# Kernel optimization log

Hardware: AMD Instinct MI355X
Metric: run time of the kernel (lower is better)

Reference implementation:

```python
import jax, jax.numpy as jnp
import numpy as np

DIM = 128

def _rope_tables(seq_len, dim, dtype):
    inv_freq = 1.0 / (10000.0 ** (jnp.arange(0, dim, 2, dtype=jnp.float32) / dim))
    t = jnp.arange(seq_len, dtype=jnp.float32)
    freqs = t[:, None] * inv_freq[None, :]          # [S, dim/2]
    emb = jnp.concatenate([freqs, freqs], axis=-1)  # [S, dim]
    return jnp.cos(emb).astype(dtype), jnp.sin(emb).astype(dtype)

def _rotate_half(x):
    x1, x2 = jnp.split(x, 2, axis=-1)
    return jnp.concatenate([-x2, x1], axis=-1)

def _apply_rope(x, cos, sin):
    return x * cos + _rotate_half(x) * sin

def setup_inputs() -> dict:
    key = jax.random.key(0)
    kq, kk, kv = jax.random.split(key, 3)
    B, S, D = 4, 4096, DIM
    return {
        "Q": jax.random.normal(kq, (B, S, D), dtype=jnp.float32),
        "K": jax.random.normal(kk, (B, S, D), dtype=jnp.float32),
        "V": jax.random.normal(kv, (B, S, D), dtype=jnp.float32),
    }

def reference(Q, K, V):
    B, S, D = Q.shape
    cos, sin = _rope_tables(S, D, Q.dtype)  # [S, D], broadcast over batch
    Qr = _apply_rope(Q, cos, sin)
    Kr = _apply_rope(K, cos, sin)
    energy = jnp.einsum('bqd,bkd->bqk', Qr, Kr)  # [B, S, S]
    # causal mask: zero out strictly-upper triangle (no softmax)
    causal = jnp.tril(jnp.ones((S, S), dtype=bool))
    energy = jnp.where(causal, energy, jnp.zeros((), dtype=energy.dtype))
    return jnp.einsum('bqk,bkd->bqd', energy, V)
```

## Files before the change

### kernel.cpp

```cpp
#include <hip/hip_runtime.h>
#include <hip/hip_bf16.h>

#define S_LEN 4096
#define DIM   128
#define NB    4
#define L_CHUNK 128
#define NCH   (S_LEN / L_CHUNK)
#define NHC   (2 * NCH)
#define ROPE_BLKS (NB * S_LEN / 4)
#define TR_BLKS   (NB * S_LEN / 64)
#define NQT   (S_LEN / 256)
#define CH_FB 3

typedef __bf16 bf16_t;
typedef __attribute__((ext_vector_type(4)))  float        f32x4;
typedef __attribute__((ext_vector_type(8)))  __bf16       bf16x8;
typedef __attribute__((ext_vector_type(16))) float        f32x16;
typedef __attribute__((ext_vector_type(4)))  unsigned int u32x4;

#define MFMA32(a, b, c) __builtin_amdgcn_mfma_f32_32x32x16_bf16((a), (b), (c), 0, 0, 0)
#define CVTPK(d, a, b) asm("v_cvt_pk_bf16_f32 %0, %1, %2" : "=v"(d) : "v"(a), "v"(b))
#define PSWAP(d, s)    asm("v_permlane32_swap_b32 %0, %1" : "+v"(d), "+v"(s))

__device__ __forceinline__ unsigned swzo(int row, int colByte) {
    return (unsigned)(row * 256 + (colByte ^ ((row & 15) << 4)));
}
__device__ __forceinline__ unsigned swz64(int row, int colByte) {
    return (unsigned)(row * 128 + (colByte ^ ((row & 7) << 4)));
}

__device__ __forceinline__ void cvt_swap(const f32x16& s, unsigned int w[8]) {
    CVTPK(w[0], s[0],  s[1]);  CVTPK(w[1], s[2],  s[3]);
    CVTPK(w[2], s[4],  s[5]);  CVTPK(w[3], s[6],  s[7]);
    CVTPK(w[4], s[8],  s[9]);  CVTPK(w[5], s[10], s[11]);
    CVTPK(w[6], s[12], s[13]); CVTPK(w[7], s[14], s[15]);
    PSWAP(w[0], w[2]); PSWAP(w[1], w[3]);
    PSWAP(w[4], w[6]); PSWAP(w[5], w[7]);
}

__launch_bounds__(256, 2)
__global__ void mega_prep_kernel(const float* __restrict__ Q,
                                 const float* __restrict__ K,
                                 const float* __restrict__ V,
                                 bf16_t* __restrict__ Qr,
                                 bf16_t* __restrict__ Kr,
                                 bf16_t* __restrict__ Vt,
                                 bf16_t* __restrict__ Gh) {
    __shared__ bf16_t KsT[128 * 64];
    __shared__ bf16_t VsT[128 * 64];
    int b  = blockIdx.x >> 6;
    int hc = blockIdx.x & 63;
    int k0 = hc * 64;
    int tid = threadIdx.x, w = tid >> 6, lane = tid & 63;
    int lr = lane & 31, lg = lane >> 5;

    {
        int srow = tid >> 2;
        int j    = tid & 3;
        int s    = k0 + srow;
        size_t base = ((size_t)b * S_LEN + s) * DIM;
        f32x4 ql[4], qh[4], kl[4], vl[4], vh[4], kh[4];
        #pragma unroll
        for (int u = 0; u < 4; ++u) {
            ql[u] = *(const f32x4*)(Q + base + 16 * j + 4 * u);
            qh[u] = *(const f32x4*)(Q + base + 64 + 16 * j + 4 * u);
            kl[u] = *(const f32x4*)(K + base + 16 * j + 4 * u);
            kh[u] = *(const f32x4*)(K + base + 64 + 16 * j + 4 * u);
            vl[u] = *(const f32x4*)(V + base + 16 * j + 4 * u);
            vh[u] = *(const f32x4*)(V + base + 64 + 16 * j + 4 * u);
        }
        bf16_t oql[16], oqh[16], okl[16], okh[16];
        #pragma unroll
        for (int e = 0; e < 16; ++e) {
            int i = 16 * j + e;
            float ex      = -(float)i * (13.287712379549449f / 64.0f);
            float inv_rev = exp2f(ex) * 0.15915494309189535f;
            float rev = (float)s * inv_rev;
            float fr  = rev - floorf(rev);
            float c  = __builtin_amdgcn_cosf(fr);
            float sn = __builtin_amdgcn_sinf(fr);
            float q1 = ql[e >> 2][e & 3], q2 = qh[e >> 2][e & 3];
            float k1 = kl[e >> 2][e & 3], k2 = kh[e >> 2][e & 3];
            oql[e] = (bf16_t)(q1 * c - q2 * sn);
            oqh[e] = (bf16_t)(q2 * c + q1 * sn);
            okl[e] = (bf16_t)(k1 * c - k2 * sn);
            okh[e] = (bf16_t)(k2 * c + k1 * sn);
        }
        #pragma unroll
        for (int hlf = 0; hlf < 2; ++hlf) {
            *(bf16x8*)(Qr + base + 16 * j + 8 * hlf)      = *(bf16x8*)&oql[8 * hlf];
            *(bf16x8*)(Qr + base + 64 + 16 * j + 8 * hlf) = *(bf16x8*)&oqh[8 * hlf];
            *(bf16x8*)(Kr + base + 16 * j + 8 * hlf)      = *(bf16x8*)&okl[8 * hlf];
            *(bf16x8*)(Kr + base + 64 + 16 * j + 8 * hlf) = *(bf16x8*)&okh[8 * hlf];
        }
        #pragma unroll
        for (int e = 0; e < 16; ++e) {
            int dk = 16 * j + e;
            *(bf16_t*)((char*)KsT + swz64(dk,      srow * 2)) = okl[e];
            *(bf16_t*)((char*)KsT + swz64(dk + 64, srow * 2)) = okh[e];
            *(bf16_t*)((char*)VsT + swz64(dk,      srow * 2)) = (bf16_t)vl[e >> 2][e & 3];
            *(bf16_t*)((char*)VsT + swz64(dk + 64, srow * 2)) = (bf16_t)vh[e >> 2][e & 3];
        }
    }
    __syncthreads();

    f32x16 acc[4];
    #pragma unroll
    for (int db = 0; db < 4; ++db)
        #pragma unroll
        for (int r = 0; r < 16; ++r) acc[db][r] = 0.f;

    #pragma unroll
    for (int sI = 0; sI < 4; ++sI) {
        bf16x8 af = *(const bf16x8*)((const char*)VsT +
            swz64(32 * w + lr, (sI * 16 + lg * 8) * 2));
        #pragma unroll
        for (int db = 0; db < 4; ++db) {
            bf16x8 bfr = *(const bf16x8*)((const char*)KsT +
                swz64(32 * db + lr, (sI * 16 + lg * 8) * 2));
            acc[db] = MFMA32(af, bfr, acc[db]);
        }
    }
    bf16_t* Gc = Gh + ((size_t)b * NHC + hc) * DIM * DIM;
    #pragma unroll
    for (int db = 0; db < 4; ++db)
        #pragma unroll
        for (int r = 0; r < 16; ++r) {
            int dv = 32 * w + (r & 3) + ((r >> 2) << 3) + (lg << 2);
            Gc[(size_t)dv * DIM + 32 * db + lr] = (bf16_t)acc[db][r];
        }

    #pragma unroll
    for (int m = 0; m < 4; ++m) {
        int idx  = tid + 256 * m;
        int dv   = idx >> 3;
        int slot = idx & 7;
        bf16x8 v = *(const bf16x8*)((const char*)VsT + swz64(dv, slot * 16));
        *(bf16x8*)(Vt + ((size_t)b * DIM + dv) * S_LEN + k0 + slot * 8) = v;
    }
}

__global__ void stage2_kernel(const bf16_t* __restrict__ Gh, bf16_t* __restrict__ Gp) {
    int b = blockIdx.x >> 6;
    int p = (blockIdx.x & 63) * 128 + threadIdx.x;
    const bf16_t* ph = Gh + (size_t)b * NHC * DIM * DIM + (size_t)p * 2;
    bf16_t* pp = Gp + (size_t)b * NCH * DIM * DIM + (size_t)p * 2;
    float rlo = 0.f, rhi = 0.f;
    #pragma unroll
    for (int c = 0; c < NCH; ++c) {
        unsigned s = (unsigned)__builtin_bit_cast(unsigned short, (bf16_t)rlo) |
                     ((unsigned)__builtin_bit_cast(unsigned short, (bf16_t)rhi) << 16);
        *(unsigned*)(pp + (size_t)c * DIM * DIM) = s;
        unsigned u0 = *(const unsigned*)(ph + (size_t)(2 * c) * DIM * DIM);
        unsigned u1 = *(const unsigned*)(ph + (size_t)(2 * c + 1) * DIM * DIM);
        rlo += __builtin_bit_cast(float, u0 << 16) + __builtin_bit_cast(float, u1 << 16);
        rhi += __builtin_bit_cast(float, u0 & 0xffff0000u) +
               __builtin_bit_cast(float, u1 & 0xffff0000u);
    }
}

__launch_bounds__(256, 1)
__global__ void stage3_kernel(const bf16_t* __restrict__ Qr,
                              const bf16_t* __restrict__ Kr,
                              const bf16_t* __restrict__ Vt,
                              const bf16_t* __restrict__ Gp,
                              float* __restrict__ Out) {
    __shared__ bf16_t Ks[128 * 128];
    __shared__ bf16_t Vs[64 * 128];
    int b  = blockIdx.x >> 6;
    int c  = (blockIdx.x >> 1) & 31;
    int dh = blockIdx.x & 1;
    int tid = threadIdx.x, w = tid >> 6, lane = tid & 63;
    int lr = lane & 31, lg = lane >> 5;
    int q0 = c * L_CHUNK;
    const bf16_t* Qb = Qr + (size_t)b * S_LEN * DIM;
    const bf16_t* Kb = Kr + (size_t)b * S_LEN * DIM;
    const bf16_t* Vb = Vt + (size_t)b * DIM * S_LEN;
    const bf16_t* Gb = Gp + ((size_t)b * NCH + c) * DIM * DIM;

    bf16x8 qf[8];
    #pragma unroll
    for (int s2 = 0; s2 < 8; ++s2)
        qf[s2] = *(const bf16x8*)(Qb + (size_t)(q0 + 32 * w + lr) * DIM
                                  + s2 * 16 + lg * 8);

    #pragma unroll
    for (int j = 0; j < 8; ++j) {
        int idx = tid + j * 256;
        int row = idx >> 4, slot = idx & 15;
        u32x4 kd = *(const u32x4*)(Kb + (size_t)(q0 + row) * DIM + slot * 8);
        *(u32x4*)((char*)Ks + swzo(row, slot * 16)) = kd;
    }
    #pragma unroll
    for (int j = 0; j < 4; ++j) {
        int idx = tid + j * 256;
        int row = idx >> 4, slot = idx & 15;
        u32x4 vd = *(const u32x4*)(Vb + (size_t)(64 * dh + row) * S_LEN + q0 + slot * 8);
        *(u32x4*)((char*)Vs + swzo(row, slot * 16)) = vd;
    }
    __syncthreads();

    f32x16 acc[2];
    #pragma unroll
    for (int i = 0; i < 2; ++i)
        #pragma unroll
        for (int r = 0; r < 16; ++r) acc[i][r] = 0.f;

    if (c > 0) {
        #pragma unroll
        for (int s2 = 0; s2 < 8; ++s2) {
            #pragma unroll
            for (int i = 0; i < 2; ++i) {
                bf16x8 gfr = *(const bf16x8*)(Gb +
                    (size_t)(64 * dh + 32 * i + lr) * DIM + s2 * 16 + lg * 8);
                acc[i] = MFMA32(qf[s2], gfr, acc[i]);
            }
        }
    }

    for (int g = 0; g <= w; ++g) {
        int ksub = g * 32;
        f32x16 sa;
        #pragma unroll
        for (int r = 0; r < 16; ++r) sa[r] = 0.f;
        #pragma unroll
        for (int s2 = 0; s2 < 8; ++s2) {
            bf16x8 af = *(const bf16x8*)((const char*)Ks +
                swzo(ksub + lr, (s2 * 16 + lg * 8) * 2));
            sa = MFMA32(af, qf[s2], sa);
        }
        if (g == w) {
            #pragma unroll
            for (int r = 0; r < 16; ++r) {
                int crow = (r & 3) + ((r >> 2) << 3) + (lg << 2);
                sa[r] = (crow > lr) ? 0.f : sa[r];
            }
        }
        unsigned int wv[8];
        cvt_swap(sa, wv);
        u32x4 tA = {wv[0], wv[1], wv[2], wv[3]};
        u32x4 tB = {wv[4], wv[5], wv[6], wv[7]};
        bf16x8 pA = __builtin_bit_cast(bf16x8, tA);
        bf16x8 pB = __builtin_bit_cast(bf16x8, tB);
        #pragma unroll
        for (int i = 0; i < 2; ++i) {
            bf16x8 v0 = *(const bf16x8*)((const char*)Vs +
                swzo(32 * i + lr, (ksub + lg * 8) * 2));
            bf16x8 v1 = *(const bf16x8*)((const char*)Vs +
                swzo(32 * i + lr, (ksub + 16 + lg * 8) * 2));
            acc[i] = MFMA32(pA, v0, acc[i]);
            acc[i] = MFMA32(pB, v1, acc[i]);
        }
    }

    float* Ob = Out + (size_t)b * S_LEN * DIM;
    #pragma unroll
    for (int i = 0; i < 2; ++i)
        #pragma unroll
        for (int r = 0; r < 16; ++r) {
            int q = q0 + 32 * w + (r & 3) + ((r >> 2) << 3) + (lg << 2);
            int d = 64 * dh + 32 * i + lr;
            Ob[(size_t)q * DIM + d] = acc[i][r];
        }
}

__global__ void prep_fb_kernel(const float* __restrict__ Q,
                               const float* __restrict__ K,
                               const float* __restrict__ V,
                               bf16_t* __restrict__ Qr,
                               bf16_t* __restrict__ Kr,
                               bf16_t* __restrict__ Vt) {
    int bid = blockIdx.x;
    int t   = threadIdx.x;
    if (bid < ROPE_BLKS) {
        int i   = t & 63;
        int row = bid * 4 + (t >> 6);
        int s   = row & (S_LEN - 1);
        size_t base = (size_t)row * DIM;
        float e       = -(float)i * (13.287712379549449f / 64.0f);
        float inv_rev = exp2f(e) * 0.15915494309189535f;
        float rev = (float)s * inv_rev;
        float fr  = rev - floorf(rev);
        float c  = __builtin_amdgcn_cosf(fr);
        float sn = __builtin_amdgcn_sinf(fr);
        float q1 = Q[base + i], q2 = Q[base + i + 64];
        float k1 = K[base + i], k2 = K[base + i + 64];
        Qr[base + i]      = (bf16_t)(q1 * c - q2 * sn);
        Qr[base + i + 64] = (bf16_t)(q2 * c + q1 * sn);
        Kr[base + i]      = (bf16_t)(k1 * c - k2 * sn);
        Kr[base + i + 64] = (bf16_t)(k2 * c + k1 * sn);
    } else {
        int idx = bid - ROPE_BLKS;
        int b   = idx >> 6;
        int s0  = (idx & 63) * 64;
        int d   = t >> 1;
        int sh  = (t & 1) * 32;
        const float* vb = V + (size_t)b * S_LEN * DIM;
        bf16_t* ob = Vt + ((size_t)b * DIM + d) * S_LEN;
        #pragma unroll
        for (int j8 = 0; j8 < 4; ++j8) {
            bf16x8 u;
            #pragma unroll
            for (int e2 = 0; e2 < 8; ++e2) {
                int s = s0 + sh + j8 * 8 + e2;
                u[e2] = (bf16_t)vb[(size_t)s * DIM + d];
            }
            *(bf16x8*)(ob + s0 + sh + j8 * 8) = u;
        }
    }
}

__launch_bounds__(256, 2)
__global__ void attn_fb_kernel(const bf16_t* __restrict__ Qr,
                               const bf16_t* __restrict__ Kr,
                               const bf16_t* __restrict__ Vt,
                               float* __restrict__ Out) {
    __shared__ bf16_t Kt[128 * 128];
    __shared__ bf16_t Vl[128 * 128];
    int b = blockIdx.x & 3;
    int t = blockIdx.x >> 2;
    int qt = 0, c0 = 0;
    for (int i2 = NQT - 1; i2 >= 0; --i2) {
        int n = (2 * (i2 + 1) + CH_FB - 1) / CH_FB;
        if (t < n) { qt = i2; c0 = t; break; }
        t -= n;
    }
    int nkt   = 2 * (qt + 1);
    int kt_lo = c0 * CH_FB;
    int kt_hi = min(kt_lo + CH_FB, nkt);
    bool single = ((nkt + CH_FB - 1) / CH_FB) == 1;

    int tid = threadIdx.x, w = tid >> 6, lane = tid & 63;
    int lr = lane & 31, lg = lane >> 5;
    int qw = qt * 256 + w * 64;
    const bf16_t* Qb = Qr + (size_t)b * S_LEN * DIM;
    const bf16_t* Kb = Kr + (size_t)b * S_LEN * DIM;
    const bf16_t* Vb = Vt + (size_t)b * DIM * S_LEN;

    bf16x8 qf[2][8];
    #pragma unroll
    for (int qb = 0; qb < 2; ++qb)
        #pragma unroll
        for (int s2 = 0; s2 < 8; ++s2)
            qf[qb][s2] = *(const bf16x8*)(Qb + (size_t)(qw + qb * 32 + lr) * DIM
                                          + s2 * 16 + lg * 8);
    f32x16 acc[2][4];
    #pragma unroll
    for (int qb = 0; qb < 2; ++qb)
        #pragma unroll
        for (int db = 0; db < 4; ++db)
            #pragma unroll
            for (int r = 0; r < 16; ++r) acc[qb][db][r] = 0.f;

    for (int kt = kt_lo; kt < kt_hi; ++kt) {
        int kbase = kt * 128;
        #pragma unroll
        for (int j = 0; j < 8; ++j) {
            int idx = tid + j * 256;
            int row = idx >> 4, slot = idx & 15;
            u32x4 kd = *(const u32x4*)(Kb + (size_t)(kbase + row) * DIM + slot * 8);
            *(u32x4*)((char*)Kt + swzo(row, slot * 16)) = kd;
            u32x4 vd = *(const u32x4*)(Vb + (size_t)row * S_LEN + kbase + slot * 8);
            *(u32x4*)((char*)Vl + swzo(row, slot * 16)) = vd;
        }
        __syncthreads();
        #pragma unroll
        for (int kb = 0; kb < 4; ++kb) {
            int ksub = kb * 32;
            int kmin = kbase + ksub;
            if (kmin > qw + 63) break;
            bool do0 = (kmin <= qw + 31);
            f32x16 s0, s1;
            #pragma unroll
            for (int r = 0; r < 16; ++r) { s0[r] = 0.f; s1[r] = 0.f; }
            #pragma unroll
            for (int h = 0; h < 2; ++h) {
                bf16x8 af[4];
                #pragma unroll
                for (int s2 = 0; s2 < 4; ++s2)
                    af[s2] = *(const bf16x8*)((const char*)Kt +
                        swzo(ksub + lr, (h * 64 + s2 * 16 + lg * 8) * 2));
                #pragma unroll
                for (int s2 = 0; s2 < 4; ++s2) {
                    if (do0) s0 = MFMA32(af[s2], qf[0][h * 4 + s2], s0);
                    s1 = MFMA32(af[s2], qf[1][h * 4 + s2], s1);
                }
            }
            if (kmin + 31 > qw) {
                #pragma unroll
                for (int r = 0; r < 16; ++r) {
                    int kg = kmin + (r & 3) + ((r >> 2) << 3) + (lg << 2);
                    s0[r] = (kg > qw + lr)      ? 0.f : s0[r];
                    s1[r] = (kg > qw + 32 + lr) ? 0.f : s1[r];
                }
            }
            unsigned int w0[8], w1[8];
            cvt_swap(s0, w0);
            cvt_swap(s1, w1);
            u32x4 t00 = {w0[0], w0[1], w0[2], w0[3]};
            u32x4 t01 = {w0[4], w0[5], w0[6], w0[7]};
            u32x4 t10 = {w1[0], w1[1], w1[2], w1[3]};
            u32x4 t11 = {w1[4], w1[5], w1[6], w1[7]};
            bf16x8 p00 = __builtin_bit_cast(bf16x8, t00);
            bf16x8 p01 = __builtin_bit_cast(bf16x8, t01);
            bf16x8 p10 = __builtin_bit_cast(bf16x8, t10);
            bf16x8 p11 = __builtin_bit_cast(bf16x8, t11);
            #pragma unroll
            for (int db = 0; db < 4; ++db) {
                bf16x8 vb0 = *(const bf16x8*)((const char*)Vl +
                    swzo(db * 32 + lr, (ksub + lg * 8) * 2));
                bf16x8 vb1 = *(const bf16x8*)((const char*)Vl +
                    swzo(db * 32 + lr, (ksub + 16 + lg * 8) * 2));
                if (do0) {
                    acc[0][db] = MFMA32(p00, vb0, acc[0][db]);
                    acc[0][db] = MFMA32(p01, vb1, acc[0][db]);
                }
                acc[1][db] = MFMA32(p10, vb0, acc[1][db]);
                acc[1][db] = MFMA32(p11, vb1, acc[1][db]);
            }
        }
        __syncthreads();
    }
    float* Ob = Out + (size_t)b * S_LEN * DIM;
    #pragma unroll
    for (int qb = 0; qb < 2; ++qb)
        #pragma unroll
        for (int db = 0; db < 4; ++db)
            #pragma unroll
            for (int r = 0; r < 16; ++r) {
                int q = qw + qb * 32 + (r & 3) + ((r >> 2) << 3) + (lg << 2);
                int d = db * 32 + lr;
                float v = acc[qb][db][r];
                float* p = Ob + (size_t)q * DIM + d;
                if (single) *p = v; else atomicAdd(p, v);
            }
}

extern "C" void kernel_launch(void* const* d_in, const int* in_sizes, int n_in,
                              void* d_out, int out_size, void* d_ws, size_t ws_size,
                              hipStream_t stream) {
    const float* Q = (const float*)d_in[0];
    const float* K = (const float*)d_in[1];
    const float* V = (const float*)d_in[2];
    float* Out = (float*)d_out;

    size_t plane  = (size_t)NB * S_LEN * DIM * sizeof(bf16_t);
    size_t ghalf  = (size_t)NB * NHC * DIM * DIM * sizeof(bf16_t);
    size_t gpre   = (size_t)NB * NCH * DIM * DIM * sizeof(bf16_t);
    char* wsb = (char*)d_ws;
    bf16_t* Qr = (bf16_t*)wsb;
    bf16_t* Kr = (bf16_t*)(wsb + plane);
    bf16_t* Vt = (bf16_t*)(wsb + 2 * plane);

    if (ws_size >= 3 * plane + ghalf + gpre) {
        bf16_t* Gh = (bf16_t*)(wsb + 3 * plane);
        bf16_t* Gp = (bf16_t*)(wsb + 3 * plane + ghalf);
        mega_prep_kernel<<<NB * NHC, 256, 0, stream>>>(Q, K, V, Qr, Kr, Vt, Gh);
        stage2_kernel<<<NB * 64, 128, 0, stream>>>(Gh, Gp);
        stage3_kernel<<<NB * NCH * 2, 256, 0, stream>>>(Qr, Kr, Vt, Gp, Out);
    } else if (ws_size >= 3 * plane) {
        hipMemsetAsync(d_out, 0, (size_t)NB * S_LEN * DIM * sizeof(float), stream);
        prep_fb_kernel<<<ROPE_BLKS + TR_BLKS, 256, 0, stream>>>(Q, K, V, Qr, Kr, Vt);
        int chunks = 0;
        for (int i = 0; i < NQT; ++i) chunks += (2 * (i + 1) + CH_FB - 1) / CH_FB;
        attn_fb_kernel<<<NB * chunks, 256, 0, stream>>>(Qr, Kr, Vt, Out);
    }
}
```

Measured before the change: 30.06 us.

## Fuse three stage kernels into one cooperative kernel with grid syncs

Merges the prep (RoPE, transpose, per-chunk KᵀV), prefix-sum and attention stages into one cooperative kernel of 256 blocks, using grid.sync between stages instead of separate launches. This removes two kernel launch gaps and tail effects. The prefix-sum stage now handles one bf16 element per thread instead of a packed pair, and launch bounds drop to one block per SM. It relies on cooperative launch support and on all 256 blocks being co-resident.

New measurement: 104.4 us. 3.47x slower.

```diff
diff --git a/kernel.cpp b/kernel.cpp
--- a/kernel.cpp
+++ b/kernel.cpp
@@ -1,5 +1,8 @@
 #include <hip/hip_runtime.h>
 #include <hip/hip_bf16.h>
+#include <hip/hip_cooperative_groups.h>
+
+namespace cg = cooperative_groups;
 
 #define S_LEN 4096
 #define DIM   128
@@ -38,230 +41,231 @@
     PSWAP(w[4], w[6]); PSWAP(w[5], w[7]);
 }
 
-__launch_bounds__(256, 2)
-__global__ void mega_prep_kernel(const float* __restrict__ Q,
+__launch_bounds__(256, 1)
+__global__ void fused_all_kernel(const float* __restrict__ Q,
                                  const float* __restrict__ K,
                                  const float* __restrict__ V,
                                  bf16_t* __restrict__ Qr,
                                  bf16_t* __restrict__ Kr,
                                  bf16_t* __restrict__ Vt,
-                                 bf16_t* __restrict__ Gh) {
-    __shared__ bf16_t KsT[128 * 64];
-    __shared__ bf16_t VsT[128 * 64];
-    int b  = blockIdx.x >> 6;
-    int hc = blockIdx.x & 63;
-    int k0 = hc * 64;
+                                 bf16_t* __restrict__ Gh,
+                                 bf16_t* __restrict__ Gp,
+                                 float* __restrict__ Out) {
+    __shared__ char smem[49152];
+    cg::grid_group grid = cg::this_grid();
+
+    int bid = blockIdx.x;
     int tid = threadIdx.x, w = tid >> 6, lane = tid & 63;
     int lr = lane & 31, lg = lane >> 5;
 
     {
-        int srow = tid >> 2;
-        int j    = tid & 3;
-        int s    = k0 + srow;
-        size_t base = ((size_t)b * S_LEN + s) * DIM;
-        f32x4 ql[4], qh[4], kl[4], vl[4], vh[4], kh[4];
-        #pragma unroll
-        for (int u = 0; u < 4; ++u) {
-            ql[u] = *(const f32x4*)(Q + base + 16 * j + 4 * u);
-            qh[u] = *(const f32x4*)(Q + base + 64 + 16 * j + 4 * u);
-            kl[u] = *(const f32x4*)(K + base + 16 * j + 4 * u);
-            kh[u] = *(const f32x4*)(K + base + 64 + 16 * j + 4 * u);
-            vl[u] = *(const f32x4*)(V + base + 16 * j + 4 * u);
-            vh[u] = *(const f32x4*)(V + base + 64 + 16 * j + 4 * u);
-        }
-        bf16_t oql[16], oqh[16], okl[16], okh[16];
-        #pragma unroll
-        for (int e = 0; e < 16; ++e) {
-            int i = 16 * j + e;
-            float ex      = -(float)i * (13.287712379549449f / 64.0f);
-            float inv_rev = exp2f(ex) * 0.15915494309189535f;
-            float rev = (float)s * inv_rev;
-            float fr  = rev - floorf(rev);
-            float c  = __builtin_amdgcn_cosf(fr);
-            float sn = __builtin_amdgcn_sinf(fr);
-            float q1 = ql[e >> 2][e & 3], q2 = qh[e >> 2][e & 3];
-            float k1 = kl[e >> 2][e & 3], k2 = kh[e >> 2][e & 3];
-            oql[e] = (bf16_t)(q1 * c - q2 * sn);
-            oqh[e] = (bf16_t)(q2 * c + q1 * sn);
-            okl[e] = (bf16_t)(k1 * c - k2 * sn);
-            okh[e] = (bf16_t)(k2 * c + k1 * sn);
-        }
-        #pragma unroll
-        for (int hlf = 0; hlf < 2; ++hlf) {
-            *(bf16x8*)(Qr + base + 16 * j + 8 * hlf)      = *(bf16x8*)&oql[8 * hlf];
-            *(bf16x8*)(Qr + base + 64 + 16 * j + 8 * hlf) = *(bf16x8*)&oqh[8 * hlf];
-            *(bf16x8*)(Kr + base + 16 * j + 8 * hlf)      = *(bf16x8*)&okl[8 * hlf];
-            *(bf16x8*)(Kr + base + 64 + 16 * j + 8 * hlf) = *(bf16x8*)&okh[8 * hlf];
-        }
-        #pragma unroll
-        for (int e = 0; e < 16; ++e) {
-            int dk = 16 * j + e;
-            *(bf16_t*)((char*)KsT + swz64(dk,      srow * 2)) = okl[e];
-            *(bf16_t*)((char*)KsT + swz64(dk + 64, srow * 2)) = okh[e];
-            *(bf16_t*)((char*)VsT + swz64(dk,      srow * 2)) = (bf16_t)vl[e >> 2][e & 3];
-            *(bf16_t*)((char*)VsT + swz64(dk + 64, srow * 2)) = (bf16_t)vh[e >> 2][e & 3];
-        }
-    }
-    __syncthreads();
-
-    f32x16 acc[4];
-    #pragma unroll
-    for (int db = 0; db < 4; ++db)
-        #pragma unroll
-        for (int r = 0; r < 16; ++r) acc[db][r] = 0.f;
-
-    #pragma unroll
-    for (int sI = 0; sI < 4; ++sI) {
-        bf16x8 af = *(const bf16x8*)((const char*)VsT +
-            swz64(32 * w + lr, (sI * 16 + lg * 8) * 2));
-        #pragma unroll
-        for (int db = 0; db < 4; ++db) {
-            bf16x8 bfr = *(const bf16x8*)((const char*)KsT +
-                swz64(32 * db + lr, (sI * 16 + lg * 8) * 2));
-            acc[db] = MFMA32(af, bfr, acc[db]);
-        }
-    }
-    bf16_t* Gc = Gh + ((size_t)b * NHC + hc) * DIM * DIM;
-    #pragma unroll
-    for (int db = 0; db < 4; ++db)
-        #pragma unroll
-        for (int r = 0; r < 16; ++r) {
-            int dv = 32 * w + (r & 3) + ((r >> 2) << 3) + (lg << 2);
-            Gc[(size_t)dv * DIM + 32 * db + lr] = (bf16_t)acc[db][r];
-        }
-
-    #pragma unroll
-    for (int m = 0; m < 4; ++m) {
-        int idx  = tid + 256 * m;
-        int dv   = idx >> 3;
-        int slot = idx & 7;
-        bf16x8 v = *(const bf16x8*)((const char*)VsT + swz64(dv, slot * 16));
-        *(bf16x8*)(Vt + ((size_t)b * DIM + dv) * S_LEN + k0 + slot * 8) = v;
-    }
-}
-
-__global__ void stage2_kernel(const bf16_t* __restrict__ Gh, bf16_t* __restrict__ Gp) {
-    int b = blockIdx.x >> 6;
-    int p = (blockIdx.x & 63) * 128 + threadIdx.x;
-    const bf16_t* ph = Gh + (size_t)b * NHC * DIM * DIM + (size_t)p * 2;
-    bf16_t* pp = Gp + (size_t)b * NCH * DIM * DIM + (size_t)p * 2;
-    float rlo = 0.f, rhi = 0.f;
-    #pragma unroll
-    for (int c = 0; c < NCH; ++c) {
-        unsigned s = (unsigned)__builtin_bit_cast(unsigned short, (bf16_t)rlo) |
-                     ((unsigned)__builtin_bit_cast(unsigned short, (bf16_t)rhi) << 16);
-        *(unsigned*)(pp + (size_t)c * DIM * DIM) = s;
-        unsigned u0 = *(const unsigned*)(ph + (size_t)(2 * c) * DIM * DIM);
-        unsigned u1 = *(const unsigned*)(ph + (size_t)(2 * c + 1) * DIM * DIM);
-        rlo += __builtin_bit_cast(float, u0 << 16) + __builtin_bit_cast(float, u1 << 16);
-        rhi += __builtin_bit_cast(float, u0 & 0xffff0000u) +
-               __builtin_bit_cast(float, u1 & 0xffff0000u);
-    }
-}
-
-__launch_bounds__(256, 1)
-__global__ void stage3_kernel(const bf16_t* __restrict__ Qr,
-                              const bf16_t* __restrict__ Kr,
-                              const bf16_t* __restrict__ Vt,
-                              const bf16_t* __restrict__ Gp,
-                              float* __restrict__ Out) {
-    __shared__ bf16_t Ks[128 * 128];
-    __shared__ bf16_t Vs[64 * 128];
-    int b  = blockIdx.x >> 6;
-    int c  = (blockIdx.x >> 1) & 31;
-    int dh = blockIdx.x & 1;
-    int tid = threadIdx.x, w = tid >> 6, lane = tid & 63;
-    int lr = lane & 31, lg = lane >> 5;
-    int q0 = c * L_CHUNK;
-    const bf16_t* Qb = Qr + (size_t)b * S_LEN * DIM;
-    const bf16_t* Kb = Kr + (size_t)b * S_LEN * DIM;
-    const bf16_t* Vb = Vt + (size_t)b * DIM * S_LEN;
-    const bf16_t* Gb = Gp + ((size_t)b * NCH + c) * DIM * DIM;
-
-    bf16x8 qf[8];
-    #pragma unroll
-    for (int s2 = 0; s2 < 8; ++s2)
-        qf[s2] = *(const bf16x8*)(Qb + (size_t)(q0 + 32 * w + lr) * DIM
-                                  + s2 * 16 + lg * 8);
-
-    #pragma unroll
-    for (int j = 0; j < 8; ++j) {
-        int idx = tid + j * 256;
-        int row = idx >> 4, slot = idx & 15;
-        u32x4 kd = *(const u32x4*)(Kb + (size_t)(q0 + row) * DIM + slot * 8);
-        *(u32x4*)((char*)Ks + swzo(row, slot * 16)) = kd;
-    }
-    #pragma unroll
-    for (int j = 0; j < 4; ++j) {
-        int idx = tid + j * 256;
-        int row = idx >> 4, slot = idx & 15;
-        u32x4 vd = *(const u32x4*)(Vb + (size_t)(64 * dh + row) * S_LEN + q0 + slot * 8);
-        *(u32x4*)((char*)Vs + swzo(row, slot * 16)) = vd;
-    }
-    __syncthreads();
-
-    f32x16 acc[2];
-    #pragma unroll
-    for (int i = 0; i < 2; ++i)
-        #pragma unroll
-        for (int r = 0; r < 16; ++r) acc[i][r] = 0.f;
-
-    if (c > 0) {
-        #pragma unroll
-        for (int s2 = 0; s2 < 8; ++s2) {
+        bf16_t* KsT = (bf16_t*)smem;
+        bf16_t* VsT = (bf16_t*)(smem + 16384);
+        int b  = bid >> 6;
+        int hc = bid & 63;
+        int k0 = hc * 64;
+        {
+            int srow = tid >> 2;
+            int j    = tid & 3;
+            int s    = k0 + srow;
+            size_t base = ((size_t)b * S_LEN + s) * DIM;
+            f32x4 ql[4], qh[4], kl[4], vl[4], vh[4], kh[4];
+            #pragma unroll
+            for (int u = 0; u < 4; ++u) {
+                ql[u] = *(const f32x4*)(Q + base + 16 * j + 4 * u);
+                qh[u] = *(const f32x4*)(Q + base + 64 + 16 * j + 4 * u);
+                kl[u] = *(const f32x4*)(K + base + 16 * j + 4 * u);
+                kh[u] = *(const f32x4*)(K + base + 64 + 16 * j + 4 * u);
+                vl[u] = *(const f32x4*)(V + base + 16 * j + 4 * u);
+                vh[u] = *(const f32x4*)(V + base + 64 + 16 * j + 4 * u);
+            }
+            bf16_t oql[16], oqh[16], okl[16], okh[16];
+            #pragma unroll
+            for (int e = 0; e < 16; ++e) {
+                int i = 16 * j + e;
+                float ex      = -(float)i * (13.287712379549449f / 64.0f);
+                float inv_rev = exp2f(ex) * 0.15915494309189535f;
+                float rev = (float)s * inv_rev;
+                float fr  = rev - floorf(rev);
+                float c  = __builtin_amdgcn_cosf(fr);
+                float sn = __builtin_amdgcn_sinf(fr);
+                float q1 = ql[e >> 2][e & 3], q2 = qh[e >> 2][e & 3];
+                float k1 = kl[e >> 2][e & 3], k2 = kh[e >> 2][e & 3];
+                oql[e] = (bf16_t)(q1 * c - q2 * sn);
+                oqh[e] = (bf16_t)(q2 * c + q1 * sn);
+                okl[e] = (bf16_t)(k1 * c - k2 * sn);
+                okh[e] = (bf16_t)(k2 * c + k1 * sn);
+            }
+            #pragma unroll
+            for (int hlf = 0; hlf < 2; ++hlf) {
+                *(bf16x8*)(Qr + base + 16 * j + 8 * hlf)      = *(bf16x8*)&oql[8 * hlf];
+                *(bf16x8*)(Qr + base + 64 + 16 * j + 8 * hlf) = *(bf16x8*)&oqh[8 * hlf];
+                *(bf16x8*)(Kr + base + 16 * j + 8 * hlf)      = *(bf16x8*)&okl[8 * hlf];
+                *(bf16x8*)(Kr + base + 64 + 16 * j + 8 * hlf) = *(bf16x8*)&okh[8 * hlf];
+            }
+            #pragma unroll
+            for (int e = 0; e < 16; ++e) {
+                int dk = 16 * j + e;
+                *(bf16_t*)((char*)KsT + swz64(dk,      srow * 2)) = okl[e];
+                *(bf16_t*)((char*)KsT + swz64(dk + 64, srow * 2)) = okh[e];
+                *(bf16_t*)((char*)VsT + swz64(dk,      srow * 2)) = (bf16_t)vl[e >> 2][e & 3];
+                *(bf16_t*)((char*)VsT + swz64(dk + 64, srow * 2)) = (bf16_t)vh[e >> 2][e & 3];
+            }
+        }
+        __syncthreads();
+
+        f32x16 acc[4];
+        #pragma unroll
+        for (int db = 0; db < 4; ++db)
+            #pragma unroll
+            for (int r = 0; r < 16; ++r) acc[db][r] = 0.f;
+
+        #pragma unroll
+        for (int sI = 0; sI < 4; ++sI) {
+            bf16x8 af = *(const bf16x8*)((const char*)VsT +
+                swz64(32 * w + lr, (sI * 16 + lg * 8) * 2));
+            #pragma unroll
+            for (int db = 0; db < 4; ++db) {
+                bf16x8 bfr = *(const bf16x8*)((const char*)KsT +
+                    swz64(32 * db + lr, (sI * 16 + lg * 8) * 2));
+                acc[db] = MFMA32(af, bfr, acc[db]);
+            }
+        }
+        bf16_t* Gc = Gh + ((size_t)b * NHC + hc) * DIM * DIM;
+        #pragma unroll
+        for (int db = 0; db < 4; ++db)
+            #pragma unroll
+            for (int r = 0; r < 16; ++r) {
+                int dv = 32 * w + (r & 3) + ((r >> 2) << 3) + (lg << 2);
+                Gc[(size_t)dv * DIM + 32 * db + lr] = (bf16_t)acc[db][r];
+            }
+
+        #pragma unroll
+        for (int m = 0; m < 4; ++m) {
+            int idx  = tid + 256 * m;
+            int dv   = idx >> 3;
+            int slot = idx & 7;
+            bf16x8 v = *(const bf16x8*)((const char*)VsT + swz64(dv, slot * 16));
+            *(bf16x8*)(Vt + ((size_t)b * DIM + dv) * S_LEN + k0 + slot * 8) = v;
+        }
+    }
+
+    grid.sync();
+
+    {
+        int col = bid * 256 + tid;
+        int b   = col >> 14;
+        int p   = col & 16383;
+        const bf16_t* ph = Gh + (size_t)b * NHC * DIM * DIM + p;
+        bf16_t* pp = Gp + (size_t)b * NCH * DIM * DIM + p;
+        float run = 0.f;
+        #pragma unroll
+        for (int c = 0; c < NCH; ++c) {
+            pp[(size_t)c * DIM * DIM] = (bf16_t)run;
+            run += (float)ph[(size_t)(2 * c) * DIM * DIM] +
+                   (float)ph[(size_t)(2 * c + 1) * DIM * DIM];
+        }
+    }
+
+    grid.sync();
+
+    {
+        bf16_t* Ks = (bf16_t*)smem;
+        bf16_t* Vs = (bf16_t*)(smem + 32768);
+        int b  = bid >> 6;
+        int c  = (bid >> 1) & 31;
+        int dh = bid & 1;
+        int q0 = c * L_CHUNK;
+        const bf16_t* Qb = Qr + (size_t)b * S_LEN * DIM;
+        const bf16_t* Kb = Kr + (size_t)b * S_LEN * DIM;
+        const bf16_t* Vb = Vt + (size_t)b * DIM * S_LEN;
+        const bf16_t* Gb = Gp + ((size_t)b * NCH + c) * DIM * DIM;
+
+        bf16x8 qf[8];
+        #pragma unroll
+        for (int s2 = 0; s2 < 8; ++s2)
+            qf[s2] = *(const bf16x8*)(Qb + (size_t)(q0 + 32 * w + lr) * DIM
+                                      + s2 * 16 + lg * 8);
+
+        #pragma unroll
+        for (int j = 0; j < 8; ++j) {
+            int idx = tid + j * 256;
+            int row = idx >> 4, slot = idx & 15;
+            u32x4 kd = *(const u32x4*)(Kb + (size_t)(q0 + row) * DIM + slot * 8);
+            *(u32x4*)((char*)Ks + swzo(row, slot * 16)) = kd;
+        }
+        #pragma unroll
+        for (int j = 0; j < 4; ++j) {
+            int idx = tid + j * 256;
+            int row = idx >> 4, slot = idx & 15;
+            u32x4 vd = *(const u32x4*)(Vb + (size_t)(64 * dh + row) * S_LEN + q0 + slot * 8);
+            *(u32x4*)((char*)Vs + swzo(row, slot * 16)) = vd;
+        }
+        __syncthreads();
+
+        f32x16 acc[2];
+        #pragma unroll
+        for (int i = 0; i < 2; ++i)
+            #pragma unroll
+            for (int r = 0; r < 16; ++r) acc[i][r] = 0.f;
+
+        if (c > 0) {
+            #pragma unroll
+            for (int s2 = 0; s2 < 8; ++s2) {
+                #pragma unroll
+                for (int i = 0; i < 2; ++i) {
+                    bf16x8 gfr = *(const bf16x8*)(Gb +
+                        (size_t)(64 * dh + 32 * i + lr) * DIM + s2 * 16 + lg * 8);
+                    acc[i] = MFMA32(qf[s2], gfr, acc[i]);
+                }
+            }
+        }
+
+        for (int g = 0; g <= w; ++g) {
+            int ksub = g * 32;
+            f32x16 sa;
+            #pragma unroll
+            for (int r = 0; r < 16; ++r) sa[r] = 0.f;
+            #pragma unroll
+            for (int s2 = 0; s2 < 8; ++s2) {
+                bf16x8 af = *(const bf16x8*)((const char*)Ks +
+                    swzo(ksub + lr, (s2 * 16 + lg * 8) * 2));
+                sa = MFMA32(af, qf[s2], sa);
+            }
+            if (g == w) {
+                #pragma unroll
+                for (int r = 0; r < 16; ++r) {
+                    int crow = (r & 3) + ((r >> 2) << 3) + (lg << 2);
+                    sa[r] = (crow > lr) ? 0.f : sa[r];
+                }
+            }
+            unsigned int wv[8];
+            cvt_swap(sa, wv);
+            u32x4 tA = {wv[0], wv[1], wv[2], wv[3]};
+            u32x4 tB = {wv[4], wv[5], wv[6], wv[7]};
+            bf16x8 pA = __builtin_bit_cast(bf16x8, tA);
+            bf16x8 pB = __builtin_bit_cast(bf16x8, tB);
             #pragma unroll
             for (int i = 0; i < 2; ++i) {
-                bf16x8 gfr = *(const bf16x8*)(Gb +
-                    (size_t)(64 * dh + 32 * i + lr) * DIM + s2 * 16 + lg * 8);
-                acc[i] = MFMA32(qf[s2], gfr, acc[i]);
-            }
-        }
-    }
-
-    for (int g = 0; g <= w; ++g) {
-        int ksub = g * 32;
-        f32x16 sa;
-        #pragma unroll
-        for (int r = 0; r < 16; ++r) sa[r] = 0.f;
-        #pragma unroll
-        for (int s2 = 0; s2 < 8; ++s2) {
-            bf16x8 af = *(const bf16x8*)((const char*)Ks +
-                swzo(ksub + lr, (s2 * 16 + lg * 8) * 2));
-            sa = MFMA32(af, qf[s2], sa);
-        }
-        if (g == w) {
+                bf16x8 v0 = *(const bf16x8*)((const char*)Vs +
+                    swzo(32 * i + lr, (ksub + lg * 8) * 2));
+                bf16x8 v1 = *(const bf16x8*)((const char*)Vs +
+                    swzo(32 * i + lr, (ksub + 16 + lg * 8) * 2));
+                acc[i] = MFMA32(pA, v0, acc[i]);
+                acc[i] = MFMA32(pB, v1, acc[i]);
+            }
+        }
+
+        float* Ob = Out + (size_t)b * S_LEN * DIM;
+        #pragma unroll
+        for (int i = 0; i < 2; ++i)
             #pragma unroll
             for (int r = 0; r < 16; ++r) {
-                int crow = (r & 3) + ((r >> 2) << 3) + (lg << 2);
-                sa[r] = (crow > lr) ? 0.f : sa[r];
-            }
-        }
-        unsigned int wv[8];
-        cvt_swap(sa, wv);
-        u32x4 tA = {wv[0], wv[1], wv[2], wv[3]};
-        u32x4 tB = {wv[4], wv[5], wv[6], wv[7]};
-        bf16x8 pA = __builtin_bit_cast(bf16x8, tA);
-        bf16x8 pB = __builtin_bit_cast(bf16x8, tB);
-        #pragma unroll
-        for (int i = 0; i < 2; ++i) {
-            bf16x8 v0 = *(const bf16x8*)((const char*)Vs +
-                swzo(32 * i + lr, (ksub + lg * 8) * 2));
-            bf16x8 v1 = *(const bf16x8*)((const char*)Vs +
-                swzo(32 * i + lr, (ksub + 16 + lg * 8) * 2));
-            acc[i] = MFMA32(pA, v0, acc[i]);
-            acc[i] = MFMA32(pB, v1, acc[i]);
-        }
-    }
-
-    float* Ob = Out + (size_t)b * S_LEN * DIM;
-    #pragma unroll
-    for (int i = 0; i < 2; ++i)
-        #pragma unroll
-        for (int r = 0; r < 16; ++r) {
-            int q = q0 + 32 * w + (r & 3) + ((r >> 2) << 3) + (lg << 2);
-            int d = 64 * dh + 32 * i + lr;
-            Ob[(size_t)q * DIM + d] = acc[i][r];
-        }
+                int q = q0 + 32 * w + (r & 3) + ((r >> 2) << 3) + (lg << 2);
+                int d = 64 * dh + 32 * i + lr;
+                Ob[(size_t)q * DIM + d] = acc[i][r];
+            }
+    }
 }
 
 __global__ void prep_fb_kernel(const float* __restrict__ Q,
@@ -455,9 +459,10 @@
     if (ws_size >= 3 * plane + ghalf + gpre) {
         bf16_t* Gh = (bf16_t*)(wsb + 3 * plane);
         bf16_t* Gp = (bf16_t*)(wsb + 3 * plane + ghalf);
-        mega_prep_kernel<<<NB * NHC, 256, 0, stream>>>(Q, K, V, Qr, Kr, Vt, Gh);
-        stage2_kernel<<<NB * 64, 128, 0, stream>>>(Gh, Gp);
-        stage3_kernel<<<NB * NCH * 2, 256, 0, stream>>>(Qr, Kr, Vt, Gp, Out);
+        void* kargs[] = {(void*)&Q, (void*)&K, (void*)&V, (void*)&Qr, (void*)&Kr,
+                         (void*)&Vt, (void*)&Gh, (void*)&Gp, (void*)&Out};
+        hipLaunchCooperativeKernel((const void*)fused_all_kernel,
+                                   dim3(NB * NHC), dim3(256), kargs, 0, stream);
     } else if (ws_size >= 3 * plane) {
         hipMemsetAsync(d_out, 0, (size_t)NB * S_LEN * DIM * sizeof(float), stream);
         prep_fb_kernel<<<ROPE_BLKS + TR_BLKS, 256, 0, stream>>>(Q, K, V, Qr, Kr, Vt);
```

## Fuse RoPE of Q/K into consumer kernels and stage prefix state in LDS

Applied to the files above, without the earlier changes.

The prep kernel no longer writes rotated bf16 Q and K planes to the workspace. Instead stage3 reads fp32 Q and K directly and applies RoPE on the fly, and the G kernel recomputes rotated K locally. This removes the round-trip writes and reads of two bf16 planes. In exchange it adds an extra fp32 read of K and Q plus duplicated sin/cos work. Stage3 also copies its prefix-state slice into swizzled LDS once, rather than reading it from global memory inside the MFMA loop, which costs extra LDS.

Measured after the change: 31.96 us. +6.3%, slower.

```diff
diff --git a/kernel.cpp b/kernel.cpp
--- a/kernel.cpp
+++ b/kernel.cpp
@@ -38,14 +38,20 @@
     PSWAP(w[4], w[6]); PSWAP(w[5], w[7]);
 }
 
+__device__ __forceinline__ void ropesc(int seq, int i, float& cc, float& ss) {
+    float ex      = -(float)i * (13.287712379549449f / 64.0f);
+    float inv_rev = exp2f(ex) * 0.15915494309189535f;
+    float rev = (float)seq * inv_rev;
+    float fr  = rev - floorf(rev);
+    cc = __builtin_amdgcn_cosf(fr);
+    ss = __builtin_amdgcn_sinf(fr);
+}
+
 __launch_bounds__(256, 2)
-__global__ void mega_prep_kernel(const float* __restrict__ Q,
-                                 const float* __restrict__ K,
-                                 const float* __restrict__ V,
-                                 bf16_t* __restrict__ Qr,
-                                 bf16_t* __restrict__ Kr,
-                                 bf16_t* __restrict__ Vt,
-                                 bf16_t* __restrict__ Gh) {
+__global__ void g_kernel(const float* __restrict__ K,
+                         const float* __restrict__ V,
+                         bf16_t* __restrict__ Vt,
+                         bf16_t* __restrict__ Gh) {
     __shared__ bf16_t KsT[128 * 64];
     __shared__ bf16_t VsT[128 * 64];
     int b  = blockIdx.x >> 6;
@@ -59,45 +65,25 @@
         int j    = tid & 3;
         int s    = k0 + srow;
         size_t base = ((size_t)b * S_LEN + s) * DIM;
-        f32x4 ql[4], qh[4], kl[4], vl[4], vh[4], kh[4];
+        f32x4 kl[4], kh[4], vl[4], vh[4];
         #pragma unroll
         for (int u = 0; u < 4; ++u) {
-            ql[u] = *(const f32x4*)(Q + base + 16 * j + 4 * u);
-            qh[u] = *(const f32x4*)(Q + base + 64 + 16 * j + 4 * u);
             kl[u] = *(const f32x4*)(K + base + 16 * j + 4 * u);
             kh[u] = *(const f32x4*)(K + base + 64 + 16 * j + 4 * u);
             vl[u] = *(const f32x4*)(V + base + 16 * j + 4 * u);
             vh[u] = *(const f32x4*)(V + base + 64 + 16 * j + 4 * u);
         }
-        bf16_t oql[16], oqh[16], okl[16], okh[16];
         #pragma unroll
         for (int e = 0; e < 16; ++e) {
             int i = 16 * j + e;
-            float ex      = -(float)i * (13.287712379549449f / 64.0f);
-            float inv_rev = exp2f(ex) * 0.15915494309189535f;
-            float rev = (float)s * inv_rev;
-            float fr  = rev - floorf(rev);
-            float c  = __builtin_amdgcn_cosf(fr);
-            float sn = __builtin_amdgcn_sinf(fr);
-            float q1 = ql[e >> 2][e & 3], q2 = qh[e >> 2][e & 3];
+            float cc, ssn;
+            ropesc(s, i, cc, ssn);
             float k1 = kl[e >> 2][e & 3], k2 = kh[e >> 2][e & 3];
-            oql[e] = (bf16_t)(q1 * c - q2 * sn);
-            oqh[e] = (bf16_t)(q2 * c + q1 * sn);
-            okl[e] = (bf16_t)(k1 * c - k2 * sn);
-            okh[e] = (bf16_t)(k2 * c + k1 * sn);
-        }
-        #pragma unroll
-        for (int hlf = 0; hlf < 2; ++hlf) {
-            *(bf16x8*)(Qr + base + 16 * j + 8 * hlf)      = *(bf16x8*)&oql[8 * hlf];
-            *(bf16x8*)(Qr + base + 64 + 16 * j + 8 * hlf) = *(bf16x8*)&oqh[8 * hlf];
-            *(bf16x8*)(Kr + base + 16 * j + 8 * hlf)      = *(bf16x8*)&okl[8 * hlf];
-            *(bf16x8*)(Kr + base + 64 + 16 * j + 8 * hlf) = *(bf16x8*)&okh[8 * hlf];
-        }
-        #pragma unroll
-        for (int e = 0; e < 16; ++e) {
-            int dk = 16 * j + e;
-            *(bf16_t*)((char*)KsT + swz64(dk,      srow * 2)) = okl[e];
-            *(bf16_t*)((char*)KsT + swz64(dk + 64, srow * 2)) = okh[e];
+            bf16_t okl = (bf16_t)(k1 * cc - k2 * ssn);
+            bf16_t okh = (bf16_t)(k2 * cc + k1 * ssn);
+            int dk = i;
+            *(bf16_t*)((char*)KsT + swz64(dk,      srow * 2)) = okl;
+            *(bf16_t*)((char*)KsT + swz64(dk + 64, srow * 2)) = okh;
             *(bf16_t*)((char*)VsT + swz64(dk,      srow * 2)) = (bf16_t)vl[e >> 2][e & 3];
             *(bf16_t*)((char*)VsT + swz64(dk + 64, srow * 2)) = (bf16_t)vh[e >> 2][e & 3];
         }
@@ -160,37 +146,75 @@
 }
 
 __launch_bounds__(256, 1)
-__global__ void stage3_kernel(const bf16_t* __restrict__ Qr,
-                              const bf16_t* __restrict__ Kr,
+__global__ void stage3_kernel(const float* __restrict__ Qf,
+                              const float* __restrict__ Kf,
                               const bf16_t* __restrict__ Vt,
                               const bf16_t* __restrict__ Gp,
                               float* __restrict__ Out) {
     __shared__ bf16_t Ks[128 * 128];
     __shared__ bf16_t Vs[64 * 128];
+    __shared__ bf16_t Gs[64 * 128];
     int b  = blockIdx.x >> 6;
     int c  = (blockIdx.x >> 1) & 31;
     int dh = blockIdx.x & 1;
     int tid = threadIdx.x, w = tid >> 6, lane = tid & 63;
     int lr = lane & 31, lg = lane >> 5;
     int q0 = c * L_CHUNK;
-    const bf16_t* Qb = Qr + (size_t)b * S_LEN * DIM;
-    const bf16_t* Kb = Kr + (size_t)b * S_LEN * DIM;
     const bf16_t* Vb = Vt + (size_t)b * DIM * S_LEN;
     const bf16_t* Gb = Gp + ((size_t)b * NCH + c) * DIM * DIM;
 
     bf16x8 qf[8];
-    #pragma unroll
-    for (int s2 = 0; s2 < 8; ++s2)
-        qf[s2] = *(const bf16x8*)(Qb + (size_t)(q0 + 32 * w + lr) * DIM
-                                  + s2 * 16 + lg * 8);
-
-    #pragma unroll
-    for (int j = 0; j < 8; ++j) {
-        int idx = tid + j * 256;
-        int row = idx >> 4, slot = idx & 15;
-        u32x4 kd = *(const u32x4*)(Kb + (size_t)(q0 + row) * DIM + slot * 8);
-        *(u32x4*)((char*)Ks + swzo(row, slot * 16)) = kd;
-    }
+    {
+        int rowg = q0 + 32 * w + lr;
+        const float* Qrow = Qf + ((size_t)b * S_LEN + rowg) * DIM;
+        #pragma unroll
+        for (int s2 = 0; s2 < 8; ++s2) {
+            int c0 = s2 * 16 + lg * 8;
+            f32x4 qa0 = *(const f32x4*)(Qrow + c0);
+            f32x4 qa1 = *(const f32x4*)(Qrow + c0 + 4);
+            f32x4 qb0 = *(const f32x4*)(Qrow + (c0 ^ 64));
+            f32x4 qb1 = *(const f32x4*)(Qrow + (c0 ^ 64) + 4);
+            float sgn = (c0 < 64) ? -1.f : 1.f;
+            bf16x8 o;
+            #pragma unroll
+            for (int e = 0; e < 8; ++e) {
+                float cc, ssn;
+                ropesc(rowg, (c0 & 63) + e, cc, ssn);
+                float qa = (e < 4) ? qa0[e & 3] : qa1[e & 3];
+                float qb = (e < 4) ? qb0[e & 3] : qb1[e & 3];
+                o[e] = (bf16_t)(qa * cc + sgn * (qb * ssn));
+            }
+            qf[s2] = o;
+        }
+    }
+
+    {
+        int row = tid >> 1, sub = tid & 1;
+        int rg  = q0 + row;
+        const float* Krow = Kf + ((size_t)b * S_LEN + rg) * DIM;
+        f32x4 klo[8], khi[8];
+        #pragma unroll
+        for (int u = 0; u < 8; ++u) {
+            klo[u] = *(const f32x4*)(Krow + 32 * sub + 4 * u);
+            khi[u] = *(const f32x4*)(Krow + 64 + 32 * sub + 4 * u);
+        }
+        #pragma unroll
+        for (int g = 0; g < 4; ++g) {
+            bf16x8 olo, ohi;
+            #pragma unroll
+            for (int e = 0; e < 8; ++e) {
+                int t = 8 * g + e;
+                float cc, ssn;
+                ropesc(rg, 32 * sub + t, cc, ssn);
+                float k1 = klo[t >> 2][t & 3], k2 = khi[t >> 2][t & 3];
+                olo[e] = (bf16_t)(k1 * cc - k2 * ssn);
+                ohi[e] = (bf16_t)(k2 * cc + k1 * ssn);
+            }
+            *(bf16x8*)((char*)Ks + swzo(row, (4 * sub + g) * 16)) = olo;
+            *(bf16x8*)((char*)Ks + swzo(row, (8 + 4 * sub + g) * 16)) = ohi;
+        }
+    }
+
     #pragma unroll
     for (int j = 0; j < 4; ++j) {
         int idx = tid + j * 256;
@@ -198,6 +222,15 @@
         u32x4 vd = *(const u32x4*)(Vb + (size_t)(64 * dh + row) * S_LEN + q0 + slot * 8);
         *(u32x4*)((char*)Vs + swzo(row, slot * 16)) = vd;
     }
+    if (c > 0) {
+        #pragma unroll
+        for (int j = 0; j < 4; ++j) {
+            int idx = tid + j * 256;
+            int row = idx >> 4, slot = idx & 15;
+            u32x4 gd = *(const u32x4*)(Gb + (size_t)(64 * dh + row) * DIM + slot * 8);
+            *(u32x4*)((char*)Gs + swzo(row, slot * 16)) = gd;
+        }
+    }
     __syncthreads();
 
     f32x16 acc[2];
@@ -211,8 +244,8 @@
         for (int s2 = 0; s2 < 8; ++s2) {
             #pragma unroll
             for (int i = 0; i < 2; ++i) {
-                bf16x8 gfr = *(const bf16x8*)(Gb +
-                    (size_t)(64 * dh + 32 * i + lr) * DIM + s2 * 16 + lg * 8);
+                bf16x8 gfr = *(const bf16x8*)((const char*)Gs +
+                    swzo(32 * i + lr, (s2 * 16 + lg * 8) * 2));
                 acc[i] = MFMA32(qf[s2], gfr, acc[i]);
             }
         }
@@ -277,18 +310,14 @@
         int row = bid * 4 + (t >> 6);
         int s   = row & (S_LEN - 1);
         size_t base = (size_t)row * DIM;
-        float e       = -(float)i * (13.287712379549449f / 64.0f);
-        float inv_rev = exp2f(e) * 0.15915494309189535f;
-        float rev = (float)s * inv_rev;
-        float fr  = rev - floorf(rev);
-        float c  = __builtin_amdgcn_cosf(fr);
-        float sn = __builtin_amdgcn_sinf(fr);
+        float cc, ssn;
+        ropesc(s, i, cc, ssn);
         float q1 = Q[base + i], q2 = Q[base + i + 64];
         float k1 = K[base + i], k2 = K[base + i + 64];
-        Qr[base + i]      = (bf16_t)(q1 * c - q2 * sn);
-        Qr[base + i + 64] = (bf16_t)(q2 * c + q1 * sn);
-        Kr[base + i]      = (bf16_t)(k1 * c - k2 * sn);
-        Kr[base + i + 64] = (bf16_t)(k2 * c + k1 * sn);
+        Qr[base + i]      = (bf16_t)(q1 * cc - q2 * ssn);
+        Qr[base + i + 64] = (bf16_t)(q2 * cc + q1 * ssn);
+        Kr[base + i]      = (bf16_t)(k1 * cc - k2 * ssn);
+        Kr[base + i + 64] = (bf16_t)(k2 * cc + k1 * ssn);
     } else {
         int idx = bid - ROPE_BLKS;
         int b   = idx >> 6;
@@ -448,17 +477,18 @@
     size_t ghalf  = (size_t)NB * NHC * DIM * DIM * sizeof(bf16_t);
     size_t gpre   = (size_t)NB * NCH * DIM * DIM * sizeof(bf16_t);
     char* wsb = (char*)d_ws;
-    bf16_t* Qr = (bf16_t*)wsb;
-    bf16_t* Kr = (bf16_t*)(wsb + plane);
-    bf16_t* Vt = (bf16_t*)(wsb + 2 * plane);
-
-    if (ws_size >= 3 * plane + ghalf + gpre) {
-        bf16_t* Gh = (bf16_t*)(wsb + 3 * plane);
-        bf16_t* Gp = (bf16_t*)(wsb + 3 * plane + ghalf);
-        mega_prep_kernel<<<NB * NHC, 256, 0, stream>>>(Q, K, V, Qr, Kr, Vt, Gh);
+
+    if (ws_size >= plane + ghalf + gpre) {
+        bf16_t* Vt = (bf16_t*)wsb;
+        bf16_t* Gh = (bf16_t*)(wsb + plane);
+        bf16_t* Gp = (bf16_t*)(wsb + plane + ghalf);
+        g_kernel<<<NB * NHC, 256, 0, stream>>>(K, V, Vt, Gh);
         stage2_kernel<<<NB * 64, 128, 0, stream>>>(Gh, Gp);
-        stage3_kernel<<<NB * NCH * 2, 256, 0, stream>>>(Qr, Kr, Vt, Gp, Out);
+        stage3_kernel<<<NB * NCH * 2, 256, 0, stream>>>(Q, K, Vt, Gp, Out);
     } else if (ws_size >= 3 * plane) {
+        bf16_t* Qr = (bf16_t*)wsb;
+        bf16_t* Kr = (bf16_t*)(wsb + plane);
+        bf16_t* Vt = (bf16_t*)(wsb + 2 * plane);
         hipMemsetAsync(d_out, 0, (size_t)NB * S_LEN * DIM * sizeof(float), stream);
         prep_fb_kernel<<<ROPE_BLKS + TR_BLKS, 256, 0, stream>>>(Q, K, V, Qr, Kr, Vt);
         int chunks = 0;
```
